# Kernel tuning notes

Hardware: AMD Instinct MI355X
Metric: run time of the kernel (lower is better)

## Reference

```python
import jax, jax.numpy as jnp
import numpy as np

NUM_HEADS = 8
OUT_DIM = 32


def setup_inputs() -> dict:
    key = jax.random.key(0)
    k1, k2, k3, k4 = jax.random.split(key, 4)
    B, N, IN = 2048, 64, 256
    h_i_list = jax.random.normal(k1, (B, N, IN), dtype=jnp.float32)
    h_j_list = jax.random.normal(k2, (B, N, IN), dtype=jnp.float32)
    # Linear weight, applied as x @ W (in_dim, num_heads*out_dim)
    W = jax.random.normal(k3, (IN, NUM_HEADS * OUT_DIM), dtype=jnp.float32) * (1.0 / np.sqrt(IN))
    W_att = jax.random.normal(k4, (1, NUM_HEADS, OUT_DIM), dtype=jnp.float32) * 0.1
    return {"h_i_list": h_i_list, "h_j_list": h_j_list, "W": W, "W_att": W_att}


def reference(h_i_list, h_j_list, W, W_att):
    B, N, _ = h_i_list.shape
    H, D = NUM_HEADS, OUT_DIM
    # [B, N, H, D]
    proj_neigh = (h_j_list @ W).reshape(B, N, H, D)
    proj_self = (h_i_list @ W).reshape(B, N, H, D)
    # attention logits: leakyReLU(sum over feature dim) -> [B, N, H]
    e_ij = jax.nn.leaky_relu(((proj_neigh + proj_self) * W_att[None]).sum(-1), 0.2)
    # softmax over neighbor dim (dim=1)
    alpha = jax.nn.softmax(e_ij, axis=1)  # [B, N, H]
    # weighted neighbor sum -> [B, H, D]
    weight_sum = jnp.einsum("bnh,bnhd->bhd", alpha, proj_neigh)
    # concat=True: [B, 1, H*D]
    h_new = weight_sum.reshape(B, 1, H * D)
    return jax.nn.elu(h_new)
```

## Files before the change

### kernel.cpp

```cpp
#include <hip/hip_runtime.h>

#define NN 64
#define IND 256
#define NH 8
#define OD 32

__device__ __forceinline__ unsigned f2bf(float f) {
  unsigned u = __float_as_uint(f);
  return (u + (((u >> 16) & 1u) + 0x7fffu)) >> 16;
}
__device__ __forceinline__ float bflo(unsigned u) { return __uint_as_float(u << 16); }
__device__ __forceinline__ float bfhi(unsigned u) { return __uint_as_float(u & 0xffff0000u); }

__global__ __launch_bounds__(256) void precompute_v(
    const float* __restrict__ W, const float* __restrict__ Watt, float* __restrict__ V) {
  int tid = blockIdx.x * 256 + threadIdx.x;
  if (tid >= IND * NH) return;
  int h = tid >> 8, k = tid & 255;
  float acc = 0.f;
#pragma unroll
  for (int d = 0; d < OD; ++d) acc += W[k * 256 + h * OD + d] * Watt[h * OD + d];
  V[h * 256 + k] = acc;
}

#define V_OFF 33792
#define E_OFF (V_OFF + 4224)
#define SMEM_BYTES (E_OFF + 2304)

__global__ __launch_bounds__(256) void gat_fused(
    const float* __restrict__ Xi, const float* __restrict__ Xj,
    const float* __restrict__ W, const float* __restrict__ V,
    float* __restrict__ out) {
  __shared__ __align__(16) unsigned char smem[SMEM_BYTES];
  unsigned* s_pk = (unsigned*)smem;
  unsigned* v_pk = (unsigned*)(smem + V_OFF);
  float* e_f = (float*)(smem + E_OFF);
  float* alpha_f = (float*)(smem + V_OFF);
  float* pp_f = (float*)(smem + V_OFF);
  float* yp_f = (float*)smem;

  const int t = threadIdx.x;
  const int b = blockIdx.x;
  const int w = t >> 6, l = t & 63;
  const int g = l >> 3, h = l & 7;

  const float4* Xi4 = (const float4*)Xi + (size_t)b * (NN * IND / 4) + w * 1024;
  const float4* Xj4 = (const float4*)Xj + (size_t)b * (NN * IND / 4) + w * 1024;

  {
    const float4* V4 = (const float4*)V;
#pragma unroll
    for (int r = 0; r < 8; ++r) {
      float4 vv = V4[r * 64 + l];
      unsigned p0 = f2bf(vv.x) | (f2bf(vv.y) << 16);
      unsigned p1 = f2bf(vv.z) | (f2bf(vv.w) << 16);
      *(uint2*)(v_pk + r * 132 + 2 * l) = make_uint2(p0, p1);
    }
  }

  float4 xj[16];
#pragma unroll
  for (int i = 0; i < 16; ++i) xj[i] = Xj4[i * 64 + l];
#pragma unroll
  for (int c = 0; c < 2; ++c) {
    float4 xi[8];
#pragma unroll
    for (int i = 0; i < 8; ++i) xi[i] = Xi4[(c * 8 + i) * 64 + l];
#pragma unroll
    for (int i = 0; i < 8; ++i) {
      int r = c * 8 + i;
      float4 a = xj[r], ci = xi[i];
      unsigned p0 = f2bf(a.x + ci.x) | (f2bf(a.y + ci.y) << 16);
      unsigned p1 = f2bf(a.z + ci.z) | (f2bf(a.w + ci.w) << 16);
      *(uint2*)(s_pk + (w * 16 + r) * 132 + l * 2) = make_uint2(p0, p1);
    }
  }

  float er[2];
#pragma unroll
  for (int pp = 0; pp < 2; ++pp) {
    int n = w * 16 + g + 8 * pp;
    const uint4* srow = (const uint4*)(s_pk + n * 132);
    const uint4* vrow = (const uint4*)(v_pk + h * 132);
    float acc = 0.f;
#pragma unroll 8
    for (int kk = 0; kk < 32; ++kk) {
      uint4 sp = srow[kk];
      uint4 vp = vrow[kk];
      acc += bflo(sp.x) * bflo(vp.x) + bfhi(sp.x) * bfhi(vp.x)
           + bflo(sp.y) * bflo(vp.y) + bfhi(sp.y) * bfhi(vp.y)
           + bflo(sp.z) * bflo(vp.z) + bfhi(sp.z) * bfhi(vp.z)
           + bflo(sp.w) * bflo(vp.w) + bfhi(sp.w) * bfhi(vp.w);
    }
    er[pp] = acc >= 0.f ? acc : 0.2f * acc;
    e_f[n * 9 + h] = er[pp];
  }
  __syncthreads();

  float m = -3.4e38f;
#pragma unroll
  for (int q = 0; q < 8; ++q) m = fmaxf(m, e_f[(g * 8 + q) * 9 + h]);
  m = fmaxf(m, __shfl_xor(m, 8, 64));
  m = fmaxf(m, __shfl_xor(m, 16, 64));
  m = fmaxf(m, __shfl_xor(m, 32, 64));
  float ssum = 0.f;
#pragma unroll
  for (int q = 0; q < 8; ++q) ssum += __expf(e_f[(g * 8 + q) * 9 + h] - m);
  ssum += __shfl_xor(ssum, 8, 64);
  ssum += __shfl_xor(ssum, 16, 64);
  ssum += __shfl_xor(ssum, 32, 64);
  float rinv = 1.f / ssum;

#pragma unroll
  for (int pp = 0; pp < 2; ++pp) {
    int n = w * 16 + g + 8 * pp;
    alpha_f[n * 8 + h] = __expf(er[pp] - m) * rinv;
  }

  float4 acc4[8];
#pragma unroll
  for (int hh = 0; hh < 8; ++hh) acc4[hh] = make_float4(0.f, 0.f, 0.f, 0.f);
#pragma unroll
  for (int i = 0; i < 16; ++i) {
    int n = w * 16 + i;
    float4 a0 = *(const float4*)(alpha_f + n * 8);
    float4 a1 = *(const float4*)(alpha_f + n * 8 + 4);
    float al[8] = {a0.x, a0.y, a0.z, a0.w, a1.x, a1.y, a1.z, a1.w};
    float4 x = xj[i];
#pragma unroll
    for (int hh = 0; hh < 8; ++hh) {
      acc4[hh].x += al[hh] * x.x;
      acc4[hh].y += al[hh] * x.y;
      acc4[hh].z += al[hh] * x.z;
      acc4[hh].w += al[hh] * x.w;
    }
  }
#pragma unroll
  for (int hh = 0; hh < 8; ++hh)
    *(float4*)(yp_f + (w * 8 + hh) * 260 + 4 * l) = acc4[hh];
  __syncthreads();

  {
    const float* ypb = yp_f + g * 260;
    const float4* W4 = (const float4*)W;
    float4 acc = make_float4(0.f, 0.f, 0.f, 0.f);
    int k0 = w * 64;
#pragma unroll 8
    for (int kk = 0; kk < 64; ++kk) {
      int k = k0 + kk;
      float yv = ypb[k] + ypb[2080 + k] + ypb[4160 + k] + ypb[6240 + k];
      float4 wv = W4[k * 64 + l];
      acc.x += yv * wv.x;
      acc.y += yv * wv.y;
      acc.z += yv * wv.z;
      acc.w += yv * wv.w;
    }
    *(float4*)(pp_f + w * 256 + 4 * l) = acc;
  }
  __syncthreads();

  {
    float s = pp_f[t] + pp_f[256 + t] + pp_f[512 + t] + pp_f[768 + t];
    out[(size_t)b * 256 + t] = s > 0.f ? s : (__expf(s) - 1.f);
  }
}

extern "C" void kernel_launch(void* const* d_in, const int* in_sizes, int n_in,
                              void* d_out, int out_size, void* d_ws, size_t ws_size,
                              hipStream_t stream) {
  const float* Xi = (const float*)d_in[0];
  const float* Xj = (const float*)d_in[1];
  const float* W = (const float*)d_in[2];
  const float* Watt = (const float*)d_in[3];
  float* out = (float*)d_out;
  float* V = (float*)d_ws;
  int B = in_sizes[0] / (NN * IND);
  precompute_v<<<(IND * NH + 255) / 256, 256, 0, stream>>>(W, Watt, V);
  gat_fused<<<B, 256, 0, stream>>>(Xi, Xj, W, V, out);
}
```

Before: 293.2 us.

## Compute attention logits with bf16 MFMA and pre-reduce partial sums before W projection

Replaces the scalar bf16-unpack dot products for the attention logits with __builtin_amdgcn_mfma_f32_16x16x32_bf16 on 16-row tiles, duplicating the 8 V rows to fill the 16-column B operand and keeping only the first 8 outputs. Adds a shared-memory pass that sums the four per-wave partial Y buffers once, so the final W projection reads one vectorized float4 of Y per four k values instead of four scalar loads per k. The costs are an extra barrier, re-reading e_f from LDS for alpha, and half of the MFMA output being wasted. The kernel is likely dominated by HBM reads of Xi and Xj, so the compute savings may have limited effect.

```diff
diff --git a/kernel.cpp b/kernel.cpp
--- a/kernel.cpp
+++ b/kernel.cpp
@@ -5,12 +5,13 @@
 #define NH 8
 #define OD 32
 
+typedef __attribute__((ext_vector_type(8))) short bf16x8;
+typedef __attribute__((ext_vector_type(4))) float f32x4;
+
 __device__ __forceinline__ unsigned f2bf(float f) {
   unsigned u = __float_as_uint(f);
   return (u + (((u >> 16) & 1u) + 0x7fffu)) >> 16;
 }
-__device__ __forceinline__ float bflo(unsigned u) { return __uint_as_float(u << 16); }
-__device__ __forceinline__ float bfhi(unsigned u) { return __uint_as_float(u & 0xffff0000u); }
 
 __global__ __launch_bounds__(256) void precompute_v(
     const float* __restrict__ W, const float* __restrict__ Watt, float* __restrict__ V) {
@@ -76,24 +77,25 @@
     }
   }
 
-  float er[2];
-#pragma unroll
-  for (int pp = 0; pp < 2; ++pp) {
-    int n = w * 16 + g + 8 * pp;
-    const uint4* srow = (const uint4*)(s_pk + n * 132);
-    const uint4* vrow = (const uint4*)(v_pk + h * 132);
-    float acc = 0.f;
-#pragma unroll 8
-    for (int kk = 0; kk < 32; ++kk) {
-      uint4 sp = srow[kk];
-      uint4 vp = vrow[kk];
-      acc += bflo(sp.x) * bflo(vp.x) + bfhi(sp.x) * bfhi(vp.x)
-           + bflo(sp.y) * bflo(vp.y) + bfhi(sp.y) * bfhi(vp.y)
-           + bflo(sp.z) * bflo(vp.z) + bfhi(sp.z) * bfhi(vp.z)
-           + bflo(sp.w) * bflo(vp.w) + bfhi(sp.w) * bfhi(vp.w);
-    }
-    er[pp] = acc >= 0.f ? acc : 0.2f * acc;
-    e_f[n * 9 + h] = er[pp];
+  {
+    const int r16 = l & 15, q = l >> 4;
+    const unsigned* arow = s_pk + (w * 16 + r16) * 132;
+    const unsigned* brow = v_pk + (r16 & 7) * 132;
+    f32x4 acc = {0.f, 0.f, 0.f, 0.f};
+#pragma unroll
+    for (int step = 0; step < 8; ++step) {
+      bf16x8 af = *(const bf16x8*)(arow + step * 16 + q * 4);
+      bf16x8 bfv = *(const bf16x8*)(brow + step * 16 + q * 4);
+      acc = __builtin_amdgcn_mfma_f32_16x16x32_bf16(af, bfv, acc, 0, 0, 0);
+    }
+    if (r16 < 8) {
+#pragma unroll
+      for (int j = 0; j < 4; ++j) {
+        float ev = acc[j];
+        ev = ev >= 0.f ? ev : 0.2f * ev;
+        e_f[(w * 16 + q * 4 + j) * 9 + r16] = ev;
+      }
+    }
   }
   __syncthreads();
 
@@ -114,7 +116,7 @@
 #pragma unroll
   for (int pp = 0; pp < 2; ++pp) {
     int n = w * 16 + g + 8 * pp;
-    alpha_f[n * 8 + h] = __expf(er[pp] - m) * rinv;
+    alpha_f[n * 8 + h] = __expf(e_f[n * 9 + h] - m) * rinv;
   }
 
   float4 acc4[8];
@@ -140,20 +142,40 @@
     *(float4*)(yp_f + (w * 8 + hh) * 260 + 4 * l) = acc4[hh];
   __syncthreads();
 
+#pragma unroll
+  for (int c = 0; c < 2; ++c) {
+    int id = t + c * 256;
+    int row = id >> 6, col = (id & 63) * 4;
+    float* p = yp_f + row * 260 + col;
+    float4 s0 = *(float4*)p;
+    float4 s1 = *(float4*)(p + 2080);
+    float4 s2 = *(float4*)(p + 4160);
+    float4 s3 = *(float4*)(p + 6240);
+    s0.x += s1.x + s2.x + s3.x;
+    s0.y += s1.y + s2.y + s3.y;
+    s0.z += s1.z + s2.z + s3.z;
+    s0.w += s1.w + s2.w + s3.w;
+    *(float4*)p = s0;
+  }
+  __syncthreads();
+
   {
     const float* ypb = yp_f + g * 260;
     const float4* W4 = (const float4*)W;
     float4 acc = make_float4(0.f, 0.f, 0.f, 0.f);
     int k0 = w * 64;
 #pragma unroll 8
-    for (int kk = 0; kk < 64; ++kk) {
-      int k = k0 + kk;
-      float yv = ypb[k] + ypb[2080 + k] + ypb[4160 + k] + ypb[6240 + k];
-      float4 wv = W4[k * 64 + l];
-      acc.x += yv * wv.x;
-      acc.y += yv * wv.y;
-      acc.z += yv * wv.z;
-      acc.w += yv * wv.w;
+    for (int kc = 0; kc < 16; ++kc) {
+      int k = k0 + kc * 4;
+      float4 yv = *(const float4*)(ypb + k);
+      float4 w0 = W4[(k + 0) * 64 + l];
+      float4 w1 = W4[(k + 1) * 64 + l];
+      float4 w2 = W4[(k + 2) * 64 + l];
+      float4 w3 = W4[(k + 3) * 64 + l];
+      acc.x += yv.x * w0.x + yv.y * w1.x + yv.z * w2.x + yv.w * w3.x;
+      acc.y += yv.x * w0.y + yv.y * w1.y + yv.z * w2.y + yv.w * w3.y;
+      acc.z += yv.x * w0.z + yv.y * w1.z + yv.z * w2.z + yv.w * w3.z;
+      acc.w += yv.x * w0.w + yv.y * w1.w + yv.z * w2.w + yv.w * w3.w;
     }
     *(float4*)(pp_f + w * 256 + 4 * l) = acc;
   }
```

Measured after the change: 285.0 us. -2.8%, faster.
